# Performance work log

Hardware: AMD Instinct MI355X
Metric: run time of the kernel (lower is better)

## Reference

```python
import jax, jax.numpy as jnp
import numpy as np

DIM = 2048
HEAD_DIM = 64
N_HEADS = 16
N_KV_HEADS = 4
RANK = 8
ALPHA = 16
LORA_SCALE = ALPHA / RANK  # 2.0
SEQ = 2048
BATCH = 1
ROPE_THETA = 10000.0


def setup_inputs() -> dict:
    key = jax.random.key(0)
    ks = jax.random.split(key, 12)
    std = 0.02
    x = jax.random.normal(ks[0], (BATCH, SEQ, DIM), dtype=jnp.float32)
    # rope tables: (SEQ, HEAD_DIM//2, 2) = (cos, sin)
    inv_freq = 1.0 / (ROPE_THETA ** (jnp.arange(0, HEAD_DIM, 2, dtype=jnp.float32) / HEAD_DIM))
    ang = jnp.arange(SEQ, dtype=jnp.float32)[:, None] * inv_freq[None, :]
    freq_cis = jnp.stack([jnp.cos(ang), jnp.sin(ang)], axis=-1)
    mk = lambda k, shp: (jax.random.normal(k, shp, dtype=jnp.float32) * std)
    return {
        "x": x,
        "freq_cis": freq_cis,
        "wq": mk(ks[1], (HEAD_DIM, DIM)),
        "wq_a": mk(ks[2], (RANK, DIM)),
        "wq_b": mk(ks[3], (N_HEADS * HEAD_DIM, RANK)),
        "wk": mk(ks[4], (HEAD_DIM, DIM)),
        "wk_a": mk(ks[5], (RANK, DIM)),
        "wk_b": mk(ks[6], (N_KV_HEADS * HEAD_DIM, RANK)),
        "wv": mk(ks[7], (HEAD_DIM, DIM)),
        "wv_a": mk(ks[8], (RANK, DIM)),
        "wv_b": mk(ks[9], (N_KV_HEADS * HEAD_DIM, RANK)),
        "wo": mk(ks[10], (DIM, HEAD_DIM)),
        "wo_share": mk(ks[11], (DIM, N_HEADS * HEAD_DIM)),
    }


def _shared_plus_lora(x, w_base, w_a, w_b, n_heads):
    # base: single head (B,S,HEAD_DIM) broadcast across heads; LoRA adds per-head delta
    base = jnp.einsum('bsd,hd->bsh', x, w_base)                    # (B,S,Dh)
    delta = jnp.einsum('bsr,or->bso', jnp.einsum('bsd,rd->bsr', x, w_a), w_b) * LORA_SCALE
    B, S, _ = x.shape
    delta = delta.reshape(B, S, n_heads, HEAD_DIM)
    return base[:, :, None, :] + delta                             # (B,S,H,Dh)


def _rope(t, freq_cis):
    # t: (B,S,H,Dh); freq_cis: (S, Dh//2, 2)
    B, S, H, D = t.shape
    tr = t.reshape(B, S, H, D // 2, 2)
    cos = freq_cis[:, None, :, 0]  # (S,1,Dh//2)
    sin = freq_cis[:, None, :, 1]
    xr, xi = tr[..., 0], tr[..., 1]
    out = jnp.stack([xr * cos - xi * sin, xr * sin + xi * cos], axis=-1)
    return out.reshape(B, S, H, D)


def reference(x, freq_cis, wq, wq_a, wq_b, wk, wk_a, wk_b, wv, wv_a, wv_b, wo, wo_share):
    B, S, _ = x.shape
    g = N_HEADS // N_KV_HEADS
    xq = _shared_plus_lora(x, wq, wq_a, wq_b, N_HEADS)      # (B,S,H,Dh)
    xk = _shared_plus_lora(x, wk, wk_a, wk_b, N_KV_HEADS)   # (B,S,Hkv,Dh)
    xv = _shared_plus_lora(x, wv, wv_a, wv_b, N_KV_HEADS)
    xq = _rope(xq, freq_cis[:S])
    xk = _rope(xk, freq_cis[:S])
    # GQA attention without materializing repeat_kv: group q heads per kv head
    q = xq.reshape(B, S, N_KV_HEADS, g, HEAD_DIM)
    scale = 1.0 / jnp.sqrt(jnp.asarray(HEAD_DIM, dtype=x.dtype))
    scores = jnp.einsum('bskgd,btkd->bkgst', q, xk) * scale  # (B,Hkv,g,S,S)
    causal = jnp.tril(jnp.ones((S, S), dtype=bool))
    scores = jnp.where(causal, scores, jnp.asarray(-jnp.inf, dtype=scores.dtype))
    p = jax.nn.softmax(scores, axis=-1)
    out = jnp.einsum('bkgst,btkd->bskgd', p, xv).reshape(B, S, N_HEADS, HEAD_DIM)
    # output projection: shared base applied per-head then summed + LoRA-style shared delta
    base = jnp.einsum('bshd,ed->bse', out, wo)
    delta = jnp.einsum('bsf,ef->bse', out.reshape(B, S, N_HEADS * HEAD_DIM), wo_share)
    return base + delta
```

## Files before the change

kernel.cpp:

```cpp
#include <hip/hip_runtime.h>
#include <hip/hip_bf16.h>

#define DEV __device__ __forceinline__

typedef unsigned short u16;
typedef __attribute__((ext_vector_type(8))) short short8;
typedef __attribute__((ext_vector_type(4))) float f32x4;
typedef __attribute__((ext_vector_type(16))) float f32x16;

DEV u16 f2bf(float f) {
  union { float f; unsigned u; } v; v.f = f;
  unsigned r = v.u + 0x7FFFu + ((v.u >> 16) & 1u);
  return (u16)(r >> 16);
}

DEV unsigned cvtpk(float lo, float hi) {
  unsigned r;
  asm("v_cvt_pk_bf16_f32 %0, %1, %2" : "=v"(r) : "v"(lo), "v"(hi));
  return r;
}

DEV void async_ld16(const u16* g, u16* l) {
  __builtin_amdgcn_global_load_lds((__attribute__((address_space(1))) void*)g,
                                   (__attribute__((address_space(3))) void*)l,
                                   16, 0, 0);
}

DEV f32x4 mfma16(short8 a, short8 b, f32x4 c) {
  return __builtin_amdgcn_mfma_f32_16x16x32_bf16(a, b, c, 0, 0, 0);
}
DEV f32x16 mfma32(short8 a, short8 b, f32x16 c) {
  return __builtin_amdgcn_mfma_f32_32x32x16_bf16(a, b, c, 0, 0, 0);
}

DEV short8 mkfrag(unsigned w0, unsigned w1, unsigned w2, unsigned w3) {
  union { unsigned u[4]; short8 s; } u;
  u.u[0] = w0; u.u[1] = w1; u.u[2] = w2; u.u[3] = w3;
  return u.s;
}

DEV short8 lds_rd(const u16* buf, int row, int colb) {
  return *(const short8*)((const char*)buf + row*128 + (colb ^ ((row & 7) << 4)));
}

#define QSCALE (0.125f * 1.4426950408889634f)

__global__ __launch_bounds__(256) void k_prep(const float* __restrict__ x,
    const float* __restrict__ wq, const float* __restrict__ wk,
    const float* __restrict__ wv, const float* __restrict__ wqa,
    const float* __restrict__ wka, const float* __restrict__ wva,
    const float* __restrict__ wo, const float* __restrict__ wos,
    u16* __restrict__ xb, u16* __restrict__ W1, u16* __restrict__ Weff) {
  const int bid = blockIdx.x;
  if (bid < 1024) {
    int i = bid*256 + threadIdx.x;
    for (; i < 1048576; i += 1024*256) {
      float4 v = ((const float4*)x)[i];
      ushort4 o;
      o.x = f2bf(v.x); o.y = f2bf(v.y); o.z = f2bf(v.z); o.w = f2bf(v.w);
      ((ushort4*)xb)[i] = o;
    }
  } else if (bid < 1280) {
    const int row = bid - 1024;
    const float* src = nullptr; float sc = 1.f;
    if (row < 64)       { src = wq  + row*2048;       sc = QSCALE; }
    else if (row < 128) { src = wk  + (row-64)*2048;  }
    else if (row < 192) { src = wv  + (row-128)*2048; }
    else if (row < 200) { src = wqa + (row-192)*2048; sc = 2.f*QSCALE; }
    else if (row < 208) { src = wka + (row-200)*2048; sc = 2.f; }
    else if (row < 216) { src = wva + (row-208)*2048; sc = 2.f; }
    for (int c = threadIdx.x; c < 2048; c += 256)
      W1[row*2048 + c] = src ? f2bf(src[c]*sc) : (u16)0;
  } else {
    const int e = bid - 1280;
    for (int f = threadIdx.x; f < 1024; f += 256)
      Weff[e*1024 + f] = f2bf(wos[e*1024 + f] + wo[e*64 + (f & 63)]);
  }
}

template<int BM, int BN>
__global__ __launch_bounds__(512)
void k_gemm_bt(const u16* __restrict__ A, const u16* __restrict__ B,
               float* __restrict__ C, int M, int N, int K, int kslice) {
  constexpr int NWC = (BN >= 128) ? 4 : 2;
  constexpr int NWR = 8 / NWC;
  constexpr int WM = BM / NWR, WN = BN / NWC;
  constexpr int FM = WM/16, FN = WN/16;
  __shared__ u16 As[BM*64];
  __shared__ u16 Bs[BN*64];
  const int tid = threadIdx.x;
  const int w = tid >> 6, l = tid & 63;
  const int wm = (w / NWC)*WM, wn = (w % NWC)*WN;
  const int tm = blockIdx.y*BM, tn = blockIdx.x*BN;
  const int k0 = blockIdx.z * kslice;
  C += (size_t)blockIdx.z * M * N;
  const int sr = (w << 3) + (l >> 3);
  const int sc = (((l & 7) ^ (l >> 3)) << 3);
  const int la = l & 15, lg = l >> 4;

  f32x4 acc[FM][FN];
#pragma unroll
  for (int i = 0; i < FM; ++i)
#pragma unroll
    for (int j = 0; j < FN; ++j) acc[i][j] = (f32x4){0.f,0.f,0.f,0.f};

  const int nk = kslice >> 6;
  for (int kt = 0; kt < nk; ++kt) {
    const int kk = k0 + (kt << 6);
#pragma unroll
    for (int j = 0; j < BM/64; ++j)
      async_ld16(A + (size_t)(tm + j*64 + sr)*K + kk + sc, &As[(j*64 + w*8)*64]);
#pragma unroll
    for (int j = 0; j < BN/64; ++j)
      async_ld16(B + (size_t)(tn + j*64 + sr)*K + kk + sc, &Bs[(j*64 + w*8)*64]);
    __syncthreads();
    short8 af[FM][2], bfr[FN][2];
#pragma unroll
    for (int mi = 0; mi < FM; ++mi)
#pragma unroll
      for (int ks = 0; ks < 2; ++ks)
        af[mi][ks] = lds_rd(As, wm + mi*16 + la, ks*64 + lg*16);
#pragma unroll
    for (int ni = 0; ni < FN; ++ni)
#pragma unroll
      for (int ks = 0; ks < 2; ++ks)
        bfr[ni][ks] = lds_rd(Bs, wn + ni*16 + la, ks*64 + lg*16);
#pragma unroll
    for (int ks = 0; ks < 2; ++ks)
#pragma unroll
      for (int mi = 0; mi < FM; ++mi)
#pragma unroll
        for (int ni = 0; ni < FN; ++ni)
          acc[mi][ni] = mfma16(af[mi][ks], bfr[ni][ks], acc[mi][ni]);
    __syncthreads();
  }
#pragma unroll
  for (int mi = 0; mi < FM; ++mi)
#pragma unroll
    for (int ni = 0; ni < FN; ++ni) {
      const int r0 = tm + wm + mi*16 + lg*4;
      const int cc = tn + wn + ni*16 + la;
#pragma unroll
      for (int r = 0; r < 4; ++r)
        C[(size_t)(r0 + r)*N + cc] = acc[mi][ni][r];
    }
}

__global__ __launch_bounds__(256)
void k_expand(const float* __restrict__ proj, const float* __restrict__ wqb,
              const float* __restrict__ wkb, const float* __restrict__ wvb,
              const float* __restrict__ freq, u16* __restrict__ Q,
              u16* __restrict__ Kb, u16* __restrict__ Vt) {
  __shared__ float prs[256];
  const int s = blockIdx.x;
  {
    const int c = threadIdx.x;
    const float* p0 = proj + s*256;
    prs[c] = (p0[c] + p0[c + 524288]) + (p0[c + 1048576] + p0[c + 1572864]);
  }
  __syncthreads();
  const int d = threadIdx.x & 63;
  const int w = threadIdx.x >> 6;
  const float cs = freq[s*64 + (d & 62)];
  const float sn = freq[s*64 + (d & 62) + 1];
#pragma unroll
  for (int pass = 0; pass < 6; ++pass) {
    const int slot = pass*4 + w;
    int bcol, tb; const float* wb;
    if (slot < 16)      { bcol = 0;   tb = 192; wb = wqb + (slot*64 + d)*8; }
    else if (slot < 20) { bcol = 64;  tb = 200; wb = wkb + ((slot-16)*64 + d)*8; }
    else                { bcol = 128; tb = 208; wb = wvb + ((slot-20)*64 + d)*8; }
    float val = prs[bcol + d];
#pragma unroll
    for (int r = 0; r < 8; ++r) val += prs[tb + r] * wb[r];
    if (slot < 20) {
      float partner = __shfl_xor(val, 1);
      val = (d & 1) ? (partner*sn + val*cs) : (val*cs - partner*sn);
    }
    u16 o = f2bf(val);
    if (slot < 16)      Q [((size_t)slot*2048 + s)*64 + d] = o;
    else if (slot < 20) Kb[((size_t)(slot-16)*2048 + s)*64 + d] = o;
    else                Vt[(size_t)(slot-20)*131072 + (size_t)d*2048 + s] = o;
  }
}

__global__ __launch_bounds__(256, 4)
void k_attn(const u16* __restrict__ Q, const u16* __restrict__ Kb,
            const u16* __restrict__ Vt, u16* __restrict__ O) {
  __shared__ float comb[3][64][33];
  __shared__ u16 scr[2048];
  const int w = threadIdx.x >> 6, l = threadIdx.x & 63;
  const int bid = blockIdx.x;
  const int h = bid & 15, kh = h >> 2;
  const int z = bid >> 4;
  const int a = z & 15, b = z >> 4;
  const int qs = (b << 4) | ((b & 1) ? (15 - a) : a);
  const int q0 = qs*32;
  const int lq = l & 31, hh = l >> 5;
  const int qg = q0 + lq;

  const u16* Qh = Q  + (size_t)h *131072;
  const u16* Kh = Kb + (size_t)kh*131072;
  const u16* Vh = Vt + (size_t)kh*131072;

  short8 bq[4];
#pragma unroll
  for (int ks = 0; ks < 4; ++ks)
    bq[ks] = *(const short8*)&Qh[qg*64 + ks*16 + hh*8];

  f32x16 acc0, acc1;
#pragma unroll
  for (int r = 0; r < 16; ++r) { acc0[r] = 0.f; acc1[r] = 0.f; }
  float lsum = 0.f;
  const float SM = 20.f;

  const int nt = (qs >> 1) + 1;

  for (int tt = w; tt < nt; tt += 4) {
    const int t0 = tt*64;
    const u16* kr0 = Kh + (size_t)(t0 + lq)*64 + hh*8;
    const u16* kr1 = kr0 + 32*64;
    short8 ak0[4], ak1[4];
#pragma unroll
    for (int ks = 0; ks < 4; ++ks) {
      ak0[ks] = *(const short8*)(kr0 + ks*16);
      ak1[ks] = *(const short8*)(kr1 + ks*16);
    }
    f32x16 s0, s1;
#pragma unroll
    for (int r = 0; r < 16; ++r) { s0[r] = 0.f; s1[r] = 0.f; }
    __builtin_amdgcn_s_setprio(1);
#pragma unroll
    for (int ks = 0; ks < 4; ++ks) {
      s0 = mfma32(ak0[ks], bq[ks], s0);
      s1 = mfma32(ak1[ks], bq[ks], s1);
    }
    __builtin_amdgcn_s_setprio(0);

    const u16* vr0 = Vh + (size_t)lq*2048 + t0 + hh*8;
    const u16* vr1 = vr0 + (size_t)32*2048;
    short8 av0[4], av1[4];
#pragma unroll
    for (int kb = 0; kb < 4; ++kb) {
      av0[kb] = *(const short8*)(vr0 + kb*16);
      av1[kb] = *(const short8*)(vr1 + kb*16);
    }

    if (t0 + 63 > q0) {
#pragma unroll
      for (int r = 0; r < 16; ++r) {
        const int tl = (r & 3) + ((r >> 2) << 3) + (hh << 2);
        if (t0 + tl > qg)      s0[r] = -1e30f;
        if (t0 + 32 + tl > qg) s1[r] = -1e30f;
      }
    }

    unsigned cwa[4][2], cwb[4][2];
    float psum = 0.f;
#pragma unroll
    for (int rq = 0; rq < 4; ++rq) {
      float a0 = exp2f(s0[4*rq+0] - SM), a1 = exp2f(s0[4*rq+1] - SM);
      float a2 = exp2f(s0[4*rq+2] - SM), a3 = exp2f(s0[4*rq+3] - SM);
      float b0 = exp2f(s1[4*rq+0] - SM), b1 = exp2f(s1[4*rq+1] - SM);
      float b2 = exp2f(s1[4*rq+2] - SM), b3 = exp2f(s1[4*rq+3] - SM);
      psum += (a0+a1) + (a2+a3) + (b0+b1) + (b2+b3);
      cwa[rq][0] = cvtpk(a0, a1); cwa[rq][1] = cvtpk(a2, a3);
      cwb[rq][0] = cvtpk(b0, b1); cwb[rq][1] = cvtpk(b2, b3);
    }
    lsum += psum;
    unsigned ya0 = __shfl_xor(hh ? cwa[0][0] : cwa[1][0], 32);
    unsigned ya1 = __shfl_xor(hh ? cwa[0][1] : cwa[1][1], 32);
    unsigned ya2 = __shfl_xor(hh ? cwa[2][0] : cwa[3][0], 32);
    unsigned ya3 = __shfl_xor(hh ? cwa[2][1] : cwa[3][1], 32);
    unsigned yb0 = __shfl_xor(hh ? cwb[0][0] : cwb[1][0], 32);
    unsigned yb1 = __shfl_xor(hh ? cwb[0][1] : cwb[1][1], 32);
    unsigned yb2 = __shfl_xor(hh ? cwb[2][0] : cwb[3][0], 32);
    unsigned yb3 = __shfl_xor(hh ? cwb[2][1] : cwb[3][1], 32);
    short8 pa0 = hh ? mkfrag(ya0, ya1, cwa[1][0], cwa[1][1])
                    : mkfrag(cwa[0][0], cwa[0][1], ya0, ya1);
    short8 pa1 = hh ? mkfrag(ya2, ya3, cwa[3][0], cwa[3][1])
                    : mkfrag(cwa[2][0], cwa[2][1], ya2, ya3);
    short8 pb0 = hh ? mkfrag(yb0, yb1, cwb[1][0], cwb[1][1])
                    : mkfrag(cwb[0][0], cwb[0][1], yb0, yb1);
    short8 pb1 = hh ? mkfrag(yb2, yb3, cwb[3][0], cwb[3][1])
                    : mkfrag(cwb[2][0], cwb[2][1], yb2, yb3);

    __builtin_amdgcn_s_setprio(1);
    acc0 = mfma32(av0[0], pa0, acc0); acc1 = mfma32(av1[0], pa0, acc1);
    acc0 = mfma32(av0[1], pa1, acc0); acc1 = mfma32(av1[1], pa1, acc1);
    acc0 = mfma32(av0[2], pb0, acc0); acc1 = mfma32(av1[2], pb0, acc1);
    acc0 = mfma32(av0[3], pb1, acc0); acc1 = mfma32(av1[3], pb1, acc1);
    __builtin_amdgcn_s_setprio(0);
  }

  if (w > 0) {
    float* cb = &comb[w-1][l][0];
#pragma unroll
    for (int r = 0; r < 16; ++r) { cb[r] = acc0[r]; cb[16+r] = acc1[r]; }
    cb[32] = lsum;
  }
  __syncthreads();
  if (w == 0) {
#pragma unroll
    for (int j = 0; j < 3; ++j) {
      const float* cb = &comb[j][l][0];
#pragma unroll
      for (int r = 0; r < 16; ++r) { acc0[r] += cb[r]; acc1[r] += cb[16+r]; }
      lsum += cb[32];
    }
    lsum += __shfl_xor(lsum, 32);
    const float inv = 1.f / lsum;
#pragma unroll
    for (int dt = 0; dt < 2; ++dt)
#pragma unroll
      for (int rq = 0; rq < 4; ++rq) {
        float v0 = (dt ? acc1[4*rq+0] : acc0[4*rq+0]) * inv;
        float v1 = (dt ? acc1[4*rq+1] : acc0[4*rq+1]) * inv;
        float v2 = (dt ? acc1[4*rq+2] : acc0[4*rq+2]) * inv;
        float v3 = (dt ? acc1[4*rq+3] : acc0[4*rq+3]) * inv;
        const int dby = dt*64 + rq*16 + hh*8;
        const int by = lq*128 + (dby ^ ((lq & 7) << 4));
        *(unsigned*)((char*)scr + by)     = cvtpk(v0, v1);
        *(unsigned*)((char*)scr + by + 4) = cvtpk(v2, v3);
      }
#pragma unroll
    for (int qq = 0; qq < 4; ++qq) {
      const int qrow = qq*8 + (l >> 3);
      const int by = qrow*128 + (((l & 7) << 4) ^ ((qrow & 7) << 4));
      short8 v = *(const short8*)((const char*)scr + by);
      *(short8*)&O[(size_t)(q0 + qrow)*1024 + h*64 + (l & 7)*8] = v;
    }
  }
}

extern "C" void kernel_launch(void* const* d_in, const int* in_sizes, int n_in,
                              void* d_out, int out_size, void* d_ws, size_t ws_size,
                              hipStream_t stream) {
  const float* x    = (const float*)d_in[0];
  const float* freq = (const float*)d_in[1];
  const float* wq   = (const float*)d_in[2];
  const float* wqa  = (const float*)d_in[3];
  const float* wqb  = (const float*)d_in[4];
  const float* wk   = (const float*)d_in[5];
  const float* wka  = (const float*)d_in[6];
  const float* wkb  = (const float*)d_in[7];
  const float* wv   = (const float*)d_in[8];
  const float* wva  = (const float*)d_in[9];
  const float* wvb  = (const float*)d_in[10];
  const float* wo   = (const float*)d_in[11];
  const float* wos  = (const float*)d_in[12];
  float* out = (float*)d_out;

  char* ws = (char*)d_ws;
  u16*  x_bf = (u16*)ws;
  u16*  Qb   = (u16*)ws;
  u16*  Kbuf = (u16*)(ws + (4u<<20));
  u16*  Vtb  = (u16*)(ws + (5u<<20));
  u16*  W1   = (u16*)(ws + (8u<<20));
  u16*  Weff = (u16*)(ws + (9u<<20));
  float* proj = (float*)(ws + (13u<<20));
  u16*  Obf  = (u16*)(ws + (13u<<20));

  k_prep    <<<3328, 256, 0, stream>>>(x, wq, wk, wv, wqa, wka, wva, wo, wos,
                                       x_bf, W1, Weff);
  k_gemm_bt<128,64><<<dim3(4,16,4), 512, 0, stream>>>(x_bf, W1, proj, 2048, 256, 2048, 512);
  k_expand  <<<dim3(2048), 256, 0, stream>>>(proj, wqb, wkb, wvb, freq, Qb, Kbuf, Vtb);
  k_attn    <<<dim3(1024), 256, 0, stream>>>(Qb, Kbuf, Vtb, Obf);
  k_gemm_bt<128,128><<<dim3(16,16,1), 512, 0, stream>>>(Obf, Weff, out, 2048, 2048, 1024, 1024);
}
```

Measured before the change: 94.32 us.

## Widen attention to 8 waves with tree reduction, deepen split-K, retile output GEMM

The attention kernel now uses 512 threads (8 waves) per block. Each wave strides over key tiles by 8, and the per-wave partial accumulators are combined with a three-level LDS tree reduction that reuses the combine buffer as output scratch. The projection GEMM splits K into 8 slices instead of 4, so k_expand now sums 8 partials. The output GEMM switches to 64x128 tiles with twice as many blocks. The aim is more parallelism and better CU fill for the causal attention and the GEMMs, at the cost of extra syncs, more LDS per block, and more partial-sum traffic.

```diff
diff --git a/kernel.cpp b/kernel.cpp
--- a/kernel.cpp
+++ b/kernel.cpp
@@ -156,7 +156,9 @@
   {
     const int c = threadIdx.x;
     const float* p0 = proj + s*256;
-    prs[c] = (p0[c] + p0[c + 524288]) + (p0[c + 1048576] + p0[c + 1572864]);
+    float t0 = (p0[c]             + p0[c +  524288]) + (p0[c + 1048576] + p0[c + 1572864]);
+    float t1 = (p0[c + 2097152] + p0[c + 2621440]) + (p0[c + 3145728] + p0[c + 3670016]);
+    prs[c] = t0 + t1;
   }
   __syncthreads();
   const int d = threadIdx.x & 63;
@@ -184,11 +186,10 @@
   }
 }
 
-__global__ __launch_bounds__(256, 4)
+__global__ __launch_bounds__(512, 8)
 void k_attn(const u16* __restrict__ Q, const u16* __restrict__ Kb,
             const u16* __restrict__ Vt, u16* __restrict__ O) {
-  __shared__ float comb[3][64][33];
-  __shared__ u16 scr[2048];
+  __shared__ float comb[4][64][33];
   const int w = threadIdx.x >> 6, l = threadIdx.x & 63;
   const int bid = blockIdx.x;
   const int h = bid & 15, kh = h >> 2;
@@ -216,7 +217,7 @@
 
   const int nt = (qs >> 1) + 1;
 
-  for (int tt = w; tt < nt; tt += 4) {
+  for (int tt = w; tt < nt; tt += 8) {
     const int t0 = tt*64;
     const u16* kr0 = Kh + (size_t)(t0 + lq)*64 + hh*8;
     const u16* kr1 = kr0 + 32*64;
@@ -293,23 +294,50 @@
     __builtin_amdgcn_s_setprio(0);
   }
 
-  if (w > 0) {
-    float* cb = &comb[w-1][l][0];
+  if (w >= 4) {
+    float* cb = &comb[w-4][l][0];
 #pragma unroll
     for (int r = 0; r < 16; ++r) { cb[r] = acc0[r]; cb[16+r] = acc1[r]; }
     cb[32] = lsum;
   }
   __syncthreads();
+  if (w < 4) {
+    const float* cb = &comb[w][l][0];
+#pragma unroll
+    for (int r = 0; r < 16; ++r) { acc0[r] += cb[r]; acc1[r] += cb[16+r]; }
+    lsum += cb[32];
+  }
+  __syncthreads();
+  if (w == 2 || w == 3) {
+    float* cb = &comb[w-2][l][0];
+#pragma unroll
+    for (int r = 0; r < 16; ++r) { cb[r] = acc0[r]; cb[16+r] = acc1[r]; }
+    cb[32] = lsum;
+  }
+  __syncthreads();
+  if (w < 2) {
+    const float* cb = &comb[w][l][0];
+#pragma unroll
+    for (int r = 0; r < 16; ++r) { acc0[r] += cb[r]; acc1[r] += cb[16+r]; }
+    lsum += cb[32];
+  }
+  __syncthreads();
+  if (w == 1) {
+    float* cb = &comb[0][l][0];
+#pragma unroll
+    for (int r = 0; r < 16; ++r) { cb[r] = acc0[r]; cb[16+r] = acc1[r]; }
+    cb[32] = lsum;
+  }
+  __syncthreads();
   if (w == 0) {
-#pragma unroll
-    for (int j = 0; j < 3; ++j) {
-      const float* cb = &comb[j][l][0];
-#pragma unroll
-      for (int r = 0; r < 16; ++r) { acc0[r] += cb[r]; acc1[r] += cb[16+r]; }
-      lsum += cb[32];
-    }
+    const float* cb = &comb[0][l][0];
+#pragma unroll
+    for (int r = 0; r < 16; ++r) { acc0[r] += cb[r]; acc1[r] += cb[16+r]; }
+    lsum += cb[32];
     lsum += __shfl_xor(lsum, 32);
     const float inv = 1.f / lsum;
+
+    u16* scr = (u16*)&comb[0][0][0];
 #pragma unroll
     for (int dt = 0; dt < 2; ++dt)
 #pragma unroll
@@ -363,8 +391,8 @@
 
   k_prep    <<<3328, 256, 0, stream>>>(x, wq, wk, wv, wqa, wka, wva, wo, wos,
                                        x_bf, W1, Weff);
-  k_gemm_bt<128,64><<<dim3(4,16,4), 512, 0, stream>>>(x_bf, W1, proj, 2048, 256, 2048, 512);
+  k_gemm_bt<128,64><<<dim3(4,16,8), 512, 0, stream>>>(x_bf, W1, proj, 2048, 256, 2048, 256);
   k_expand  <<<dim3(2048), 256, 0, stream>>>(proj, wqb, wkb, wvb, freq, Qb, Kbuf, Vtb);
-  k_attn    <<<dim3(1024), 256, 0, stream>>>(Qb, Kbuf, Vtb, Obf);
-  k_gemm_bt<128,128><<<dim3(16,16,1), 512, 0, stream>>>(Obf, Weff, out, 2048, 2048, 1024, 1024);
-}
+  k_attn    <<<dim3(1024), 512, 0, stream>>>(Qb, Kbuf, Vtb, Obf);
+  k_gemm_bt<64,128><<<dim3(16,32,1), 512, 0, stream>>>(Obf, Weff, out, 2048, 2048, 1024, 1024);
+}
```

Result: slower. 173.8 us (+84.3%).
